# Kernel tuning notes

Measured on AMD Instinct MI355X. Metric: run time of the kernel, lower is better.

## Reference

```python
import jax, jax.numpy as jnp
import numpy as np

N = 4096        # nodes
E = 131072      # edges (avg degree 32)
IN_F = 256      # in_features
OUT_F = 64      # out_features per head
H = 8           # num_heads


def setup_inputs() -> dict:
    key = jax.random.key(0)
    k1, k2, k3, k4 = jax.random.split(key, 4)
    x = jax.random.normal(k1, (N, IN_F), dtype=jnp.float32)
    # xavier-ish scales for the learned params
    W = jax.random.normal(k2, (IN_F, OUT_F * H), dtype=jnp.float32) * 0.06
    a = jax.random.normal(k3, (2 * OUT_F, 1), dtype=jnp.float32) * 0.12
    edge_index = jax.random.randint(k4, (2, E), 0, N, dtype=jnp.int32)
    return {"x": x, "W": W, "a": a, "edge_index": edge_index}


def reference(x, W, a, edge_index):
    n = x.shape[0]
    Wh = (x @ W).reshape(n, H, OUT_F)          # [N, H, F]
    src, dst = edge_index[0], edge_index[1]
    # edge score: cat(Wh[src], Wh[dst]) @ a == Wh[src]@a1 + Wh[dst]@a2
    a1 = a[:OUT_F, 0]                           # [F]
    a2 = a[OUT_F:2 * OUT_F, 0]                  # [F]
    alpha_src = Wh @ a1                         # [N, H]
    alpha_dst = Wh @ a2                         # [N, H]
    edge_e = jax.nn.leaky_relu(alpha_src[src] + alpha_dst[dst], 0.2)  # [E, H]
    # dense scatter exactly as the original module (non-edges stay 0 in softmax)
    attention = jnp.zeros((n, n, H), dtype=x.dtype).at[src, dst].set(edge_e)
    attention = jax.nn.softmax(attention, axis=1)
    # dropout is identity in eval mode
    h_prime = jnp.einsum('nmh,mhf->nhf', attention, Wh)  # [N, H, F]
    return h_prime.reshape(n, H * OUT_F)        # concat=True
```

## Files before the change

### kernel.cpp

```cpp
#include <hip/hip_runtime.h>
#include <hip/hip_bf16.h>

constexpr int NN    = 4096;
constexpr int EE    = 131072;
constexpr int IN_F  = 256;
constexpr int OUT_F = 64;
constexpr int HH    = 8;
constexpr int HF    = OUT_F * HH;
constexpr int CAP   = 128;

__device__ __forceinline__ unsigned short f2b(float f) {
    unsigned int u = __float_as_uint(f);
    u = u + 0x7FFFu + ((u >> 16) & 1u);
    return (unsigned short)(u >> 16);
}
__device__ __forceinline__ float b2f(unsigned int lo16) {
    return __uint_as_float(lo16 << 16);
}

#define TM 64
#define TN 64
#define TK 32

__global__ __launch_bounds__(256) void gemm_fused(const float* __restrict__ x,
                                                  const float* __restrict__ W,
                                                  const float* __restrict__ a,
                                                  unsigned short* __restrict__ Whb,
                                                  float* __restrict__ asrc,
                                                  float* __restrict__ adst,
                                                  float* __restrict__ S) {
    __shared__ float As[TK][TM + 4];
    __shared__ float Bs[TK][TN + 4];
    __shared__ float Scol[TN];
    int t  = threadIdx.x;
    int tx = t & 15;
    int ty = t >> 4;
    int m0 = blockIdx.x * TM;
    int n0 = blockIdx.y * TN;
    float acc[4][4] = {};

    float4 pa[2], pb[2];
    {
#pragma unroll
        for (int i = 0; i < 2; ++i) {
            int flat = i * 256 + t, row = flat >> 3, c4 = flat & 7;
            pa[i] = *(const float4*)(x + (size_t)(m0 + row) * IN_F + c4 * 4);
        }
#pragma unroll
        for (int i = 0; i < 2; ++i) {
            int flat = i * 256 + t, row = flat >> 4, c4 = flat & 15;
            pb[i] = *(const float4*)(W + (size_t)row * HF + n0 + c4 * 4);
        }
    }

    for (int k0 = 0; k0 < IN_F; k0 += TK) {
#pragma unroll
        for (int i = 0; i < 2; ++i) {
            int flat = i * 256 + t, row = flat >> 3, c4 = flat & 7;
            As[c4 * 4 + 0][row] = pa[i].x;
            As[c4 * 4 + 1][row] = pa[i].y;
            As[c4 * 4 + 2][row] = pa[i].z;
            As[c4 * 4 + 3][row] = pa[i].w;
        }
#pragma unroll
        for (int i = 0; i < 2; ++i) {
            int flat = i * 256 + t, row = flat >> 4, c4 = flat & 15;
            *(float4*)(&Bs[row][c4 * 4]) = pb[i];
        }
        __syncthreads();
        if (k0 + TK < IN_F) {
            int kn = k0 + TK;
#pragma unroll
            for (int i = 0; i < 2; ++i) {
                int flat = i * 256 + t, row = flat >> 3, c4 = flat & 7;
                pa[i] = *(const float4*)(x + (size_t)(m0 + row) * IN_F + kn + c4 * 4);
            }
#pragma unroll
            for (int i = 0; i < 2; ++i) {
                int flat = i * 256 + t, row = flat >> 4, c4 = flat & 15;
                pb[i] = *(const float4*)(W + (size_t)(kn + row) * HF + n0 + c4 * 4);
            }
        }
#pragma unroll
        for (int k = 0; k < TK; ++k) {
            float4 a4 = *(const float4*)(&As[k][ty * 4]);
            float4 b4 = *(const float4*)(&Bs[k][tx * 4]);
            float av[4] = {a4.x, a4.y, a4.z, a4.w};
            float bv[4] = {b4.x, b4.y, b4.z, b4.w};
#pragma unroll
            for (int ii = 0; ii < 4; ++ii)
#pragma unroll
                for (int jj = 0; jj < 4; ++jj)
                    acc[ii][jj] += av[ii] * bv[jj];
        }
        __syncthreads();
    }

#pragma unroll
    for (int ii = 0; ii < 4; ++ii) {
        ushort4 v;
        v.x = f2b(acc[ii][0]);
        v.y = f2b(acc[ii][1]);
        v.z = f2b(acc[ii][2]);
        v.w = f2b(acc[ii][3]);
        *(ushort4*)(Whb + (size_t)(m0 + ty * 4 + ii) * HF + n0 + tx * 4) = v;
    }

    int h = n0 >> 6;
    float a1v[4], a2v[4];
#pragma unroll
    for (int jj = 0; jj < 4; ++jj) {
        int f = tx * 4 + jj;
        a1v[jj] = a[f];
        a2v[jj] = a[OUT_F + f];
    }
#pragma unroll
    for (int ii = 0; ii < 4; ++ii) {
        float p1 = 0.f, p2 = 0.f;
#pragma unroll
        for (int jj = 0; jj < 4; ++jj) {
            p1 += acc[ii][jj] * a1v[jj];
            p2 += acc[ii][jj] * a2v[jj];
        }
#pragma unroll
        for (int mask = 1; mask < 16; mask <<= 1) {
            p1 += __shfl_xor(p1, mask);
            p2 += __shfl_xor(p2, mask);
        }
        if (tx == 0) {
            int node = m0 + ty * 4 + ii;
            asrc[node * HH + h] = p1;
            adst[node * HH + h] = p2;
        }
    }

    if (t < TN) Scol[t] = 0.f;
    __syncthreads();
#pragma unroll
    for (int jj = 0; jj < 4; ++jj) {
        float cs = acc[0][jj] + acc[1][jj] + acc[2][jj] + acc[3][jj];
        atomicAdd(&Scol[tx * 4 + jj], cs);
    }
    __syncthreads();
    if (t < TN) atomicAdd(&S[n0 + t], Scol[t]);
}

__global__ __launch_bounds__(256) void scatter_lite(const int* __restrict__ src,
                                                    const int* __restrict__ dst,
                                                    int* __restrict__ cnt,
                                                    int* __restrict__ csr_dst) {
    int e = blockIdx.x * 256 + threadIdx.x;
    if (e >= EE) return;
    int s = src[e], d = dst[e];
    int pos = atomicAdd(&cnt[s], 1);
    csr_dst[(s << 7) + pos] = d;
}

__global__ __launch_bounds__(512) void aggregate_kernel(const unsigned short* __restrict__ Whb,
                                                        const float* __restrict__ asrc,
                                                        const float* __restrict__ adst,
                                                        const float* __restrict__ S,
                                                        const int* __restrict__ cnt,
                                                        const int* __restrict__ csr_dst,
                                                        float* __restrict__ out) {
    __shared__ int           midx[CAP];
    __shared__ unsigned char dupf[CAP];
    __shared__ float         wbuf[CAP * HH];
    __shared__ float         as_sh[HH];
    __shared__ float         denom[HH];
    __shared__ float         red[8][HF];
    int i = blockIdx.x;
    int t = threadIdx.x;
    int deg = cnt[i];
    if (deg > CAP) deg = CAP;

    if (t < HH) as_sh[t] = asrc[i * HH + t];
    for (int j = t; j < deg; j += 512) midx[j] = csr_dst[(i << 7) + j];
    __syncthreads();

    for (int j = t; j < deg; j += 512) {
        int m = midx[j];
        unsigned char f = 0;
        for (int k = 0; k < j; ++k)
            if (midx[k] == m) { f = 1; break; }
        dupf[j] = f;
    }
    __syncthreads();

    for (int idx = t; idx < deg * HH; idx += 512) {
        int sl = idx >> 3, h = idx & 7;
        float w = 0.f;
        if (!dupf[sl]) {
            float xv = as_sh[h] + adst[midx[sl] * HH + h];
            xv = (xv > 0.f) ? xv : 0.2f * xv;
            w = __expf(xv) - 1.f;
        }
        wbuf[idx] = w;
    }
    __syncthreads();

    if (t < 128) {
        int h = t >> 4, ln = t & 15;
        float p = 0.f;
        for (int sl = ln; sl < deg; sl += 16) p += wbuf[sl * HH + h];
#pragma unroll
        for (int mask = 1; mask < 16; mask <<= 1) p += __shfl_xor(p, mask);
        if (ln == 0) denom[h] = (float)NN + p;
    }
    __syncthreads();

    int g = t >> 6;
    int r = t & 63;
    int h = r >> 3;
    float accv[8] = {};

    int j = g;
    uint4 uC = {0, 0, 0, 0};
    float wC = 0.f;
    if (j < deg) {
        wC = wbuf[j * HH + h];
        uC = *(const uint4*)(Whb + ((size_t)midx[j] << 9) + (r << 3));
    }
    while (j < deg) {
        int jn = j + 8;
        uint4 uN = {0, 0, 0, 0};
        float wN = 0.f;
        if (jn < deg) {
            wN = wbuf[jn * HH + h];
            uN = *(const uint4*)(Whb + ((size_t)midx[jn] << 9) + (r << 3));
        }
        accv[0] += wC * b2f(uC.x & 0xFFFFu);
        accv[1] += wC * b2f(uC.x >> 16);
        accv[2] += wC * b2f(uC.y & 0xFFFFu);
        accv[3] += wC * b2f(uC.y >> 16);
        accv[4] += wC * b2f(uC.z & 0xFFFFu);
        accv[5] += wC * b2f(uC.z >> 16);
        accv[6] += wC * b2f(uC.w & 0xFFFFu);
        accv[7] += wC * b2f(uC.w >> 16);
        uC = uN; wC = wN; j = jn;
    }

    float4 v0 = {accv[0], accv[1], accv[2], accv[3]};
    float4 v1 = {accv[4], accv[5], accv[6], accv[7]};
    *(float4*)(&red[g][r * 8])     = v0;
    *(float4*)(&red[g][r * 8 + 4]) = v1;
    __syncthreads();

    float tot = S[t];
#pragma unroll
    for (int gg = 0; gg < 8; ++gg) tot += red[gg][t];
    out[((size_t)i << 9) + t] = tot / denom[t >> 6];
}

extern "C" void kernel_launch(void* const* d_in, const int* in_sizes, int n_in,
                              void* d_out, int out_size, void* d_ws, size_t ws_size,
                              hipStream_t stream) {
    const float* x  = (const float*)d_in[0];
    const float* W  = (const float*)d_in[1];
    const float* a  = (const float*)d_in[2];
    const int*   ei = (const int*)d_in[3];
    const int* src = ei;
    const int* dst = ei + EE;
    float* out = (float*)d_out;

    char* ws = (char*)d_ws;
    unsigned short* Whb = (unsigned short*)(ws + 0);
    float* asrc     = (float*)(ws + 4194304);
    float* adst     = (float*)(ws + 4325376);
    int*   csr_dst  = (int*)  (ws + 4456448);
    float* S        = (float*)(ws + 6553600);
    int*   cnt      = (int*)  (ws + 6555648);

    hipMemsetAsync(ws + 6553600, 0, 2048 + 16384, stream);

    scatter_lite<<<EE / 256, 256, 0, stream>>>(src, dst, cnt, csr_dst);

    gemm_fused<<<dim3(NN / TM, HF / TN), 256, 0, stream>>>(x, W, a, Whb, asrc, adst, S);

    aggregate_kernel<<<NN, 512, 0, stream>>>(Whb, asrc, adst, S, cnt, csr_dst, out);
}
```

Before: 132.3 us.

## Fuse memset, scatter, GEMM and aggregation into one cooperative persistent kernel

Replaces the memset plus three separate kernel launches with a single cooperative kernel of 512 blocks × 256 threads that uses grid-wide syncs between phases: zeroing, CSR scatter, the fused GEMM, and the per-node aggregation. The aggregation phase becomes a persistent loop where each block handles 8 nodes with 4 gather groups instead of 8. This removes launch gaps and inter-kernel overhead. In exchange it adds grid barrier costs, and the aggregation gets less parallelism per node and fewer concurrent waves to hide gather latency.

Result: slower. 320.4 us (+142.3%).

```diff
diff --git a/kernel.cpp b/kernel.cpp
--- a/kernel.cpp
+++ b/kernel.cpp
@@ -1,5 +1,8 @@
 #include <hip/hip_runtime.h>
 #include <hip/hip_bf16.h>
+#include <hip/hip_cooperative_groups.h>
+
+namespace cg = cooperative_groups;
 
 constexpr int NN    = 4096;
 constexpr int EE    = 131072;
@@ -9,6 +12,9 @@
 constexpr int HF    = OUT_F * HH;
 constexpr int CAP   = 128;
 
+constexpr int GRID  = 512;
+constexpr int BLK   = 256;
+
 __device__ __forceinline__ unsigned short f2b(float f) {
     unsigned int u = __float_as_uint(f);
     u = u + 0x7FFFu + ((u >> 16) & 1u);
@@ -22,25 +28,45 @@
 #define TN 64
 #define TK 32
 
-__global__ __launch_bounds__(256) void gemm_fused(const float* __restrict__ x,
-                                                  const float* __restrict__ W,
-                                                  const float* __restrict__ a,
-                                                  unsigned short* __restrict__ Whb,
-                                                  float* __restrict__ asrc,
-                                                  float* __restrict__ adst,
-                                                  float* __restrict__ S) {
-    __shared__ float As[TK][TM + 4];
-    __shared__ float Bs[TK][TN + 4];
-    __shared__ float Scol[TN];
-    int t  = threadIdx.x;
-    int tx = t & 15;
-    int ty = t >> 4;
-    int m0 = blockIdx.x * TM;
-    int n0 = blockIdx.y * TN;
-    float acc[4][4] = {};
-
-    float4 pa[2], pb[2];
+__global__ __launch_bounds__(BLK) void gat_mega(const float* __restrict__ x,
+                                                const float* __restrict__ W,
+                                                const float* __restrict__ a,
+                                                const int* __restrict__ src,
+                                                const int* __restrict__ dst,
+                                                unsigned short* __restrict__ Whb,
+                                                float* __restrict__ asrc,
+                                                float* __restrict__ adst,
+                                                float* __restrict__ S,
+                                                int* __restrict__ cnt,
+                                                int* __restrict__ csr_dst,
+                                                float* __restrict__ out) {
+    cg::grid_group grid = cg::this_grid();
+    int b = blockIdx.x;
+    int t = threadIdx.x;
+    int gt = b * BLK + t;
+
+    if (gt < NN) cnt[gt] = 0;
+    if (gt >= NN && gt < NN + HF) S[gt - NN] = 0.f;
+    grid.sync();
+
     {
+        int s = src[gt], d = dst[gt];
+        int pos = atomicAdd(&cnt[s], 1);
+        csr_dst[(s << 7) + pos] = d;
+    }
+    grid.sync();
+
+    {
+        __shared__ float As[TK][TM + 4];
+        __shared__ float Bs[TK][TN + 4];
+        __shared__ float Scol[TN];
+        int tx = t & 15;
+        int ty = t >> 4;
+        int m0 = (b >> 3) * TM;
+        int n0 = (b & 7) * TN;
+        float acc[4][4] = {};
+
+        float4 pa[2], pb[2];
 #pragma unroll
         for (int i = 0; i < 2; ++i) {
             int flat = i * 256 + t, row = flat >> 3, c4 = flat & 7;
@@ -51,205 +77,191 @@
             int flat = i * 256 + t, row = flat >> 4, c4 = flat & 15;
             pb[i] = *(const float4*)(W + (size_t)row * HF + n0 + c4 * 4);
         }
-    }
-
-    for (int k0 = 0; k0 < IN_F; k0 += TK) {
-#pragma unroll
-        for (int i = 0; i < 2; ++i) {
-            int flat = i * 256 + t, row = flat >> 3, c4 = flat & 7;
-            As[c4 * 4 + 0][row] = pa[i].x;
-            As[c4 * 4 + 1][row] = pa[i].y;
-            As[c4 * 4 + 2][row] = pa[i].z;
-            As[c4 * 4 + 3][row] = pa[i].w;
-        }
-#pragma unroll
-        for (int i = 0; i < 2; ++i) {
-            int flat = i * 256 + t, row = flat >> 4, c4 = flat & 15;
-            *(float4*)(&Bs[row][c4 * 4]) = pb[i];
-        }
-        __syncthreads();
-        if (k0 + TK < IN_F) {
-            int kn = k0 + TK;
+
+        for (int k0 = 0; k0 < IN_F; k0 += TK) {
 #pragma unroll
             for (int i = 0; i < 2; ++i) {
                 int flat = i * 256 + t, row = flat >> 3, c4 = flat & 7;
-                pa[i] = *(const float4*)(x + (size_t)(m0 + row) * IN_F + kn + c4 * 4);
+                As[c4 * 4 + 0][row] = pa[i].x;
+                As[c4 * 4 + 1][row] = pa[i].y;
+                As[c4 * 4 + 2][row] = pa[i].z;
+                As[c4 * 4 + 3][row] = pa[i].w;
             }
 #pragma unroll
             for (int i = 0; i < 2; ++i) {
                 int flat = i * 256 + t, row = flat >> 4, c4 = flat & 15;
-                pb[i] = *(const float4*)(W + (size_t)(kn + row) * HF + n0 + c4 * 4);
-            }
-        }
-#pragma unroll
-        for (int k = 0; k < TK; ++k) {
-            float4 a4 = *(const float4*)(&As[k][ty * 4]);
-            float4 b4 = *(const float4*)(&Bs[k][tx * 4]);
-            float av[4] = {a4.x, a4.y, a4.z, a4.w};
-            float bv[4] = {b4.x, b4.y, b4.z, b4.w};
-#pragma unroll
-            for (int ii = 0; ii < 4; ++ii)
-#pragma unroll
-                for (int jj = 0; jj < 4; ++jj)
-                    acc[ii][jj] += av[ii] * bv[jj];
-        }
+                *(float4*)(&Bs[row][c4 * 4]) = pb[i];
+            }
+            __syncthreads();
+            if (k0 + TK < IN_F) {
+                int kn = k0 + TK;
+#pragma unroll
+                for (int i = 0; i < 2; ++i) {
+                    int flat = i * 256 + t, row = flat >> 3, c4 = flat & 7;
+                    pa[i] = *(const float4*)(x + (size_t)(m0 + row) * IN_F + kn + c4 * 4);
+                }
+#pragma unroll
+                for (int i = 0; i < 2; ++i) {
+                    int flat = i * 256 + t, row = flat >> 4, c4 = flat & 15;
+                    pb[i] = *(const float4*)(W + (size_t)(kn + row) * HF + n0 + c4 * 4);
+                }
+            }
+#pragma unroll
+            for (int k = 0; k < TK; ++k) {
+                float4 a4 = *(const float4*)(&As[k][ty * 4]);
+                float4 b4 = *(const float4*)(&Bs[k][tx * 4]);
+                float av[4] = {a4.x, a4.y, a4.z, a4.w};
+                float bv[4] = {b4.x, b4.y, b4.z, b4.w};
+#pragma unroll
+                for (int ii = 0; ii < 4; ++ii)
+#pragma unroll
+                    for (int jj = 0; jj < 4; ++jj)
+                        acc[ii][jj] += av[ii] * bv[jj];
+            }
+            __syncthreads();
+        }
+
+#pragma unroll
+        for (int ii = 0; ii < 4; ++ii) {
+            ushort4 v;
+            v.x = f2b(acc[ii][0]);
+            v.y = f2b(acc[ii][1]);
+            v.z = f2b(acc[ii][2]);
+            v.w = f2b(acc[ii][3]);
+            *(ushort4*)(Whb + (size_t)(m0 + ty * 4 + ii) * HF + n0 + tx * 4) = v;
+        }
+
+        int h = n0 >> 6;
+        float a1v[4], a2v[4];
+#pragma unroll
+        for (int jj = 0; jj < 4; ++jj) {
+            int f = tx * 4 + jj;
+            a1v[jj] = a[f];
+            a2v[jj] = a[OUT_F + f];
+        }
+#pragma unroll
+        for (int ii = 0; ii < 4; ++ii) {
+            float p1 = 0.f, p2 = 0.f;
+#pragma unroll
+            for (int jj = 0; jj < 4; ++jj) {
+                p1 += acc[ii][jj] * a1v[jj];
+                p2 += acc[ii][jj] * a2v[jj];
+            }
+#pragma unroll
+            for (int mask = 1; mask < 16; mask <<= 1) {
+                p1 += __shfl_xor(p1, mask);
+                p2 += __shfl_xor(p2, mask);
+            }
+            if (tx == 0) {
+                int node = m0 + ty * 4 + ii;
+                asrc[node * HH + h] = p1;
+                adst[node * HH + h] = p2;
+            }
+        }
+
+        if (t < TN) Scol[t] = 0.f;
         __syncthreads();
+#pragma unroll
+        for (int jj = 0; jj < 4; ++jj) {
+            float cs = acc[0][jj] + acc[1][jj] + acc[2][jj] + acc[3][jj];
+            atomicAdd(&Scol[tx * 4 + jj], cs);
+        }
+        __syncthreads();
+        if (t < TN) atomicAdd(&S[n0 + t], Scol[t]);
     }
-
-#pragma unroll
-    for (int ii = 0; ii < 4; ++ii) {
-        ushort4 v;
-        v.x = f2b(acc[ii][0]);
-        v.y = f2b(acc[ii][1]);
-        v.z = f2b(acc[ii][2]);
-        v.w = f2b(acc[ii][3]);
-        *(ushort4*)(Whb + (size_t)(m0 + ty * 4 + ii) * HF + n0 + tx * 4) = v;
+    grid.sync();
+
+    {
+        __shared__ int           midx[CAP];
+        __shared__ unsigned char dupf[CAP];
+        __shared__ float         wbuf[CAP * HH];
+        __shared__ float         as_sh[HH];
+        __shared__ float         denom[HH];
+        __shared__ float         red[4][HF];
+
+        for (int i = b; i < NN; i += GRID) {
+            int deg = cnt[i];
+            if (deg > CAP) deg = CAP;
+
+            if (t < HH) as_sh[t] = asrc[i * HH + t];
+            for (int j = t; j < deg; j += BLK) midx[j] = csr_dst[(i << 7) + j];
+            __syncthreads();
+
+            for (int j = t; j < deg; j += BLK) {
+                int m = midx[j];
+                unsigned char f = 0;
+                for (int k = 0; k < j; ++k)
+                    if (midx[k] == m) { f = 1; break; }
+                dupf[j] = f;
+            }
+            __syncthreads();
+
+            for (int idx = t; idx < deg * HH; idx += BLK) {
+                int sl = idx >> 3, h = idx & 7;
+                float w = 0.f;
+                if (!dupf[sl]) {
+                    float xv = as_sh[h] + adst[midx[sl] * HH + h];
+                    xv = (xv > 0.f) ? xv : 0.2f * xv;
+                    w = __expf(xv) - 1.f;
+                }
+                wbuf[idx] = w;
+            }
+            __syncthreads();
+
+            if (t < 128) {
+                int h = t >> 4, ln = t & 15;
+                float p = 0.f;
+                for (int sl = ln; sl < deg; sl += 16) p += wbuf[sl * HH + h];
+#pragma unroll
+                for (int mask = 1; mask < 16; mask <<= 1) p += __shfl_xor(p, mask);
+                if (ln == 0) denom[h] = (float)NN + p;
+            }
+            __syncthreads();
+
+            int g = t >> 6;
+            int r = t & 63;
+            int h = r >> 3;
+            float accv[8] = {};
+
+            int j = g;
+            uint4 uC = {0, 0, 0, 0};
+            float wC = 0.f;
+            if (j < deg) {
+                wC = wbuf[j * HH + h];
+                uC = *(const uint4*)(Whb + ((size_t)midx[j] << 9) + (r << 3));
+            }
+            while (j < deg) {
+                int jn = j + 4;
+                uint4 uN = {0, 0, 0, 0};
+                float wN = 0.f;
+                if (jn < deg) {
+                    wN = wbuf[jn * HH + h];
+                    uN = *(const uint4*)(Whb + ((size_t)midx[jn] << 9) + (r << 3));
+                }
+                accv[0] += wC * b2f(uC.x & 0xFFFFu);
+                accv[1] += wC * b2f(uC.x >> 16);
+                accv[2] += wC * b2f(uC.y & 0xFFFFu);
+                accv[3] += wC * b2f(uC.y >> 16);
+                accv[4] += wC * b2f(uC.z & 0xFFFFu);
+                accv[5] += wC * b2f(uC.z >> 16);
+                accv[6] += wC * b2f(uC.w & 0xFFFFu);
+                accv[7] += wC * b2f(uC.w >> 16);
+                uC = uN; wC = wN; j = jn;
+            }
+
+            float4 v0 = {accv[0], accv[1], accv[2], accv[3]};
+            float4 v1 = {accv[4], accv[5], accv[6], accv[7]};
+            *(float4*)(&red[g][r * 8])     = v0;
+            *(float4*)(&red[g][r * 8 + 4]) = v1;
+            __syncthreads();
+
+            for (int o = t; o < HF; o += BLK) {
+                float tot = S[o] + red[0][o] + red[1][o] + red[2][o] + red[3][o];
+                out[((size_t)i << 9) + o] = tot / denom[o >> 6];
+            }
+            __syncthreads();
+        }
     }
-
-    int h = n0 >> 6;
-    float a1v[4], a2v[4];
-#pragma unroll
-    for (int jj = 0; jj < 4; ++jj) {
-        int f = tx * 4 + jj;
-        a1v[jj] = a[f];
-        a2v[jj] = a[OUT_F + f];
-    }
-#pragma unroll
-    for (int ii = 0; ii < 4; ++ii) {
-        float p1 = 0.f, p2 = 0.f;
-#pragma unroll
-        for (int jj = 0; jj < 4; ++jj) {
-            p1 += acc[ii][jj] * a1v[jj];
-            p2 += acc[ii][jj] * a2v[jj];
-        }
-#pragma unroll
-        for (int mask = 1; mask < 16; mask <<= 1) {
-            p1 += __shfl_xor(p1, mask);
-            p2 += __shfl_xor(p2, mask);
-        }
-        if (tx == 0) {
-            int node = m0 + ty * 4 + ii;
-            asrc[node * HH + h] = p1;
-            adst[node * HH + h] = p2;
-        }
-    }
-
-    if (t < TN) Scol[t] = 0.f;
-    __syncthreads();
-#pragma unroll
-    for (int jj = 0; jj < 4; ++jj) {
-        float cs = acc[0][jj] + acc[1][jj] + acc[2][jj] + acc[3][jj];
-        atomicAdd(&Scol[tx * 4 + jj], cs);
-    }
-    __syncthreads();
-    if (t < TN) atomicAdd(&S[n0 + t], Scol[t]);
-}
-
-__global__ __launch_bounds__(256) void scatter_lite(const int* __restrict__ src,
-                                                    const int* __restrict__ dst,
-                                                    int* __restrict__ cnt,
-                                                    int* __restrict__ csr_dst) {
-    int e = blockIdx.x * 256 + threadIdx.x;
-    if (e >= EE) return;
-    int s = src[e], d = dst[e];
-    int pos = atomicAdd(&cnt[s], 1);
-    csr_dst[(s << 7) + pos] = d;
-}
-
-__global__ __launch_bounds__(512) void aggregate_kernel(const unsigned short* __restrict__ Whb,
-                                                        const float* __restrict__ asrc,
-                                                        const float* __restrict__ adst,
-                                                        const float* __restrict__ S,
-                                                        const int* __restrict__ cnt,
-                                                        const int* __restrict__ csr_dst,
-                                                        float* __restrict__ out) {
-    __shared__ int           midx[CAP];
-    __shared__ unsigned char dupf[CAP];
-    __shared__ float         wbuf[CAP * HH];
-    __shared__ float         as_sh[HH];
-    __shared__ float         denom[HH];
-    __shared__ float         red[8][HF];
-    int i = blockIdx.x;
-    int t = threadIdx.x;
-    int deg = cnt[i];
-    if (deg > CAP) deg = CAP;
-
-    if (t < HH) as_sh[t] = asrc[i * HH + t];
-    for (int j = t; j < deg; j += 512) midx[j] = csr_dst[(i << 7) + j];
-    __syncthreads();
-
-    for (int j = t; j < deg; j += 512) {
-        int m = midx[j];
-        unsigned char f = 0;
-        for (int k = 0; k < j; ++k)
-            if (midx[k] == m) { f = 1; break; }
-        dupf[j] = f;
-    }
-    __syncthreads();
-
-    for (int idx = t; idx < deg * HH; idx += 512) {
-        int sl = idx >> 3, h = idx & 7;
-        float w = 0.f;
-        if (!dupf[sl]) {
-            float xv = as_sh[h] + adst[midx[sl] * HH + h];
-            xv = (xv > 0.f) ? xv : 0.2f * xv;
-            w = __expf(xv) - 1.f;
-        }
-        wbuf[idx] = w;
-    }
-    __syncthreads();
-
-    if (t < 128) {
-        int h = t >> 4, ln = t & 15;
-        float p = 0.f;
-        for (int sl = ln; sl < deg; sl += 16) p += wbuf[sl * HH + h];
-#pragma unroll
-        for (int mask = 1; mask < 16; mask <<= 1) p += __shfl_xor(p, mask);
-        if (ln == 0) denom[h] = (float)NN + p;
-    }
-    __syncthreads();
-
-    int g = t >> 6;
-    int r = t & 63;
-    int h = r >> 3;
-    float accv[8] = {};
-
-    int j = g;
-    uint4 uC = {0, 0, 0, 0};
-    float wC = 0.f;
-    if (j < deg) {
-        wC = wbuf[j * HH + h];
-        uC = *(const uint4*)(Whb + ((size_t)midx[j] << 9) + (r << 3));
-    }
-    while (j < deg) {
-        int jn = j + 8;
-        uint4 uN = {0, 0, 0, 0};
-        float wN = 0.f;
-        if (jn < deg) {
-            wN = wbuf[jn * HH + h];
-            uN = *(const uint4*)(Whb + ((size_t)midx[jn] << 9) + (r << 3));
-        }
-        accv[0] += wC * b2f(uC.x & 0xFFFFu);
-        accv[1] += wC * b2f(uC.x >> 16);
-        accv[2] += wC * b2f(uC.y & 0xFFFFu);
-        accv[3] += wC * b2f(uC.y >> 16);
-        accv[4] += wC * b2f(uC.z & 0xFFFFu);
-        accv[5] += wC * b2f(uC.z >> 16);
-        accv[6] += wC * b2f(uC.w & 0xFFFFu);
-        accv[7] += wC * b2f(uC.w >> 16);
-        uC = uN; wC = wN; j = jn;
-    }
-
-    float4 v0 = {accv[0], accv[1], accv[2], accv[3]};
-    float4 v1 = {accv[4], accv[5], accv[6], accv[7]};
-    *(float4*)(&red[g][r * 8])     = v0;
-    *(float4*)(&red[g][r * 8 + 4]) = v1;
-    __syncthreads();
-
-    float tot = S[t];
-#pragma unroll
-    for (int gg = 0; gg < 8; ++gg) tot += red[gg][t];
-    out[((size_t)i << 9) + t] = tot / denom[t >> 6];
 }
 
 extern "C" void kernel_launch(void* const* d_in, const int* in_sizes, int n_in,
@@ -271,11 +283,9 @@
     float* S        = (float*)(ws + 6553600);
     int*   cnt      = (int*)  (ws + 6555648);
 
-    hipMemsetAsync(ws + 6553600, 0, 2048 + 16384, stream);
-
-    scatter_lite<<<EE / 256, 256, 0, stream>>>(src, dst, cnt, csr_dst);
-
-    gemm_fused<<<dim3(NN / TM, HF / TN), 256, 0, stream>>>(x, W, a, Whb, asrc, adst, S);
-
-    aggregate_kernel<<<NN, 512, 0, stream>>>(Whb, asrc, adst, S, cnt, csr_dst, out);
-}
+    void* args[] = {(void*)&x, (void*)&W, (void*)&a, (void*)&src, (void*)&dst,
+                    (void*)&Whb, (void*)&asrc, (void*)&adst, (void*)&S,
+                    (void*)&cnt, (void*)&csr_dst, (void*)&out};
+    hipLaunchCooperativeKernel((const void*)gat_mega, dim3(GRID), dim3(BLK),
+                               args, 0, stream);
+}
```

## Fuse edge scatter into GEMM kernel and double-buffer shared tiles

Applied to the files above, without the earlier changes.

Merges the separate CSR-scatter kernel into the projection GEMM, so each of the 512 GEMM blocks also handles 256 edges, which removes one kernel launch. The GEMM's shared-memory tiles are now double-buffered, which drops one barrier per k-step. The cost is double the LDS usage, which may reduce occupancy. The fused grid only works because blocks times threads exactly equals the edge count.

New measurement: 128.3 us. 3.0% less time.

```diff
diff --git a/kernel.cpp b/kernel.cpp
--- a/kernel.cpp
+++ b/kernel.cpp
@@ -22,54 +22,66 @@
 #define TN 64
 #define TK 32
 
-__global__ __launch_bounds__(256) void gemm_fused(const float* __restrict__ x,
-                                                  const float* __restrict__ W,
-                                                  const float* __restrict__ a,
-                                                  unsigned short* __restrict__ Whb,
-                                                  float* __restrict__ asrc,
-                                                  float* __restrict__ adst,
-                                                  float* __restrict__ S) {
-    __shared__ float As[TK][TM + 4];
-    __shared__ float Bs[TK][TN + 4];
+__global__ __launch_bounds__(256) void gemm_scatter(const float* __restrict__ x,
+                                                    const float* __restrict__ W,
+                                                    const float* __restrict__ a,
+                                                    const int* __restrict__ src,
+                                                    const int* __restrict__ dst,
+                                                    int* __restrict__ cnt,
+                                                    int* __restrict__ csr_dst,
+                                                    unsigned short* __restrict__ Whb,
+                                                    float* __restrict__ asrc,
+                                                    float* __restrict__ adst,
+                                                    float* __restrict__ S) {
+    __shared__ float As[2][TK][TM + 4];
+    __shared__ float Bs[2][TK][TN + 4];
     __shared__ float Scol[TN];
-    int t  = threadIdx.x;
+    int b = blockIdx.x;
+    int t = threadIdx.x;
+
+    {
+        int e = b * 256 + t;
+        int s = src[e], d = dst[e];
+        int pos = atomicAdd(&cnt[s], 1);
+        csr_dst[(s << 7) + pos] = d;
+    }
+
     int tx = t & 15;
     int ty = t >> 4;
-    int m0 = blockIdx.x * TM;
-    int n0 = blockIdx.y * TN;
+    int m0 = (b >> 3) * TM;
+    int n0 = (b & 7) * TN;
     float acc[4][4] = {};
-
     float4 pa[2], pb[2];
-    {
-#pragma unroll
-        for (int i = 0; i < 2; ++i) {
-            int flat = i * 256 + t, row = flat >> 3, c4 = flat & 7;
-            pa[i] = *(const float4*)(x + (size_t)(m0 + row) * IN_F + c4 * 4);
-        }
-#pragma unroll
-        for (int i = 0; i < 2; ++i) {
-            int flat = i * 256 + t, row = flat >> 4, c4 = flat & 15;
-            pb[i] = *(const float4*)(W + (size_t)row * HF + n0 + c4 * 4);
-        }
-    }
-
-    for (int k0 = 0; k0 < IN_F; k0 += TK) {
-#pragma unroll
-        for (int i = 0; i < 2; ++i) {
-            int flat = i * 256 + t, row = flat >> 3, c4 = flat & 7;
-            As[c4 * 4 + 0][row] = pa[i].x;
-            As[c4 * 4 + 1][row] = pa[i].y;
-            As[c4 * 4 + 2][row] = pa[i].z;
-            As[c4 * 4 + 3][row] = pa[i].w;
-        }
-#pragma unroll
-        for (int i = 0; i < 2; ++i) {
-            int flat = i * 256 + t, row = flat >> 4, c4 = flat & 15;
-            *(float4*)(&Bs[row][c4 * 4]) = pb[i];
-        }
-        __syncthreads();
-        if (k0 + TK < IN_F) {
-            int kn = k0 + TK;
+
+#pragma unroll
+    for (int i = 0; i < 2; ++i) {
+        int flat = i * 256 + t, row = flat >> 3, c4 = flat & 7;
+        pa[i] = *(const float4*)(x + (size_t)(m0 + row) * IN_F + c4 * 4);
+    }
+#pragma unroll
+    for (int i = 0; i < 2; ++i) {
+        int flat = i * 256 + t, row = flat >> 4, c4 = flat & 15;
+        pb[i] = *(const float4*)(W + (size_t)row * HF + n0 + c4 * 4);
+    }
+#pragma unroll
+    for (int i = 0; i < 2; ++i) {
+        int flat = i * 256 + t, row = flat >> 3, c4 = flat & 7;
+        As[0][c4 * 4 + 0][row] = pa[i].x;
+        As[0][c4 * 4 + 1][row] = pa[i].y;
+        As[0][c4 * 4 + 2][row] = pa[i].z;
+        As[0][c4 * 4 + 3][row] = pa[i].w;
+    }
+#pragma unroll
+    for (int i = 0; i < 2; ++i) {
+        int flat = i * 256 + t, row = flat >> 4, c4 = flat & 15;
+        *(float4*)(&Bs[0][row][c4 * 4]) = pb[i];
+    }
+    __syncthreads();
+
+    for (int s8 = 0; s8 < 8; ++s8) {
+        int cur = s8 & 1;
+        if (s8 < 7) {
+            int kn = (s8 + 1) * TK;
 #pragma unroll
             for (int i = 0; i < 2; ++i) {
                 int flat = i * 256 + t, row = flat >> 3, c4 = flat & 7;
@@ -83,8 +95,8 @@
         }
 #pragma unroll
         for (int k = 0; k < TK; ++k) {
-            float4 a4 = *(const float4*)(&As[k][ty * 4]);
-            float4 b4 = *(const float4*)(&Bs[k][tx * 4]);
+            float4 a4 = *(const float4*)(&As[cur][k][ty * 4]);
+            float4 b4 = *(const float4*)(&Bs[cur][k][tx * 4]);
             float av[4] = {a4.x, a4.y, a4.z, a4.w};
             float bv[4] = {b4.x, b4.y, b4.z, b4.w};
 #pragma unroll
@@ -93,7 +105,23 @@
                 for (int jj = 0; jj < 4; ++jj)
                     acc[ii][jj] += av[ii] * bv[jj];
         }
-        __syncthreads();
+        if (s8 < 7) {
+            int nxt = cur ^ 1;
+#pragma unroll
+            for (int i = 0; i < 2; ++i) {
+                int flat = i * 256 + t, row = flat >> 3, c4 = flat & 7;
+                As[nxt][c4 * 4 + 0][row] = pa[i].x;
+                As[nxt][c4 * 4 + 1][row] = pa[i].y;
+                As[nxt][c4 * 4 + 2][row] = pa[i].z;
+                As[nxt][c4 * 4 + 3][row] = pa[i].w;
+            }
+#pragma unroll
+            for (int i = 0; i < 2; ++i) {
+                int flat = i * 256 + t, row = flat >> 4, c4 = flat & 15;
+                *(float4*)(&Bs[nxt][row][c4 * 4]) = pb[i];
+            }
+            __syncthreads();
+        }
     }
 
 #pragma unroll
@@ -143,17 +171,6 @@
     }
     __syncthreads();
     if (t < TN) atomicAdd(&S[n0 + t], Scol[t]);
-}
-
-__global__ __launch_bounds__(256) void scatter_lite(const int* __restrict__ src,
-                                                    const int* __restrict__ dst,
-                                                    int* __restrict__ cnt,
-                                                    int* __restrict__ csr_dst) {
-    int e = blockIdx.x * 256 + threadIdx.x;
-    if (e >= EE) return;
-    int s = src[e], d = dst[e];
-    int pos = atomicAdd(&cnt[s], 1);
-    csr_dst[(s << 7) + pos] = d;
 }
 
 __global__ __launch_bounds__(512) void aggregate_kernel(const unsigned short* __restrict__ Whb,
@@ -273,9 +290,8 @@
 
     hipMemsetAsync(ws + 6553600, 0, 2048 + 16384, stream);
 
-    scatter_lite<<<EE / 256, 256, 0, stream>>>(src, dst, cnt, csr_dst);
-
-    gemm_fused<<<dim3(NN / TM, HF / TN), 256, 0, stream>>>(x, W, a, Whb, asrc, adst, S);
+    gemm_scatter<<<512, 256, 0, stream>>>(x, W, a, src, dst, cnt, csr_dst,
+                                          Whb, asrc, adst, S);
 
     aggregate_kernel<<<NN, 512, 0, stream>>>(Whb, asrc, adst, S, cnt, csr_dst, out);
 }
```

## Use split-bf16 MFMA GEMM with preconversion and fuse edge scatter into GEMM

Applied to the files above, without the earlier changes.

Replaces the fp32 SIMT GEMM with bf16 MFMA instructions, splitting x and W into hi/lo bf16 parts (three MFMAs per tile) to keep near-fp32 accuracy. A new preconvert kernel does the hi/lo split, transposes W, and zeroes the counters, which replaces the memset. The CSR edge scatter moves into the GEMM kernel, so one launch goes away. The cost is the extra passes that write and read the converted copies, plus the scatter atomics now running inside the GEMM blocks.

Result: faster. 119.1 us (-9.9%).

```diff
diff --git a/kernel.cpp b/kernel.cpp
--- a/kernel.cpp
+++ b/kernel.cpp
@@ -9,6 +9,9 @@
 constexpr int HF    = OUT_F * HH;
 constexpr int CAP   = 128;
 
+typedef __attribute__((ext_vector_type(8))) short bf16x8;
+typedef __attribute__((ext_vector_type(4))) float f32x4;
+
 __device__ __forceinline__ unsigned short f2b(float f) {
     unsigned int u = __float_as_uint(f);
     u = u + 0x7FFFu + ((u >> 16) & 1u);
@@ -18,142 +21,161 @@
     return __uint_as_float(lo16 << 16);
 }
 
-#define TM 64
-#define TN 64
-#define TK 32
-
-__global__ __launch_bounds__(256) void gemm_fused(const float* __restrict__ x,
+__global__ __launch_bounds__(256) void preconvert(const float* __restrict__ x,
                                                   const float* __restrict__ W,
-                                                  const float* __restrict__ a,
-                                                  unsigned short* __restrict__ Whb,
-                                                  float* __restrict__ asrc,
-                                                  float* __restrict__ adst,
-                                                  float* __restrict__ S) {
-    __shared__ float As[TK][TM + 4];
-    __shared__ float Bs[TK][TN + 4];
-    __shared__ float Scol[TN];
-    int t  = threadIdx.x;
-    int tx = t & 15;
-    int ty = t >> 4;
-    int m0 = blockIdx.x * TM;
-    int n0 = blockIdx.y * TN;
-    float acc[4][4] = {};
-
-    float4 pa[2], pb[2];
+                                                  unsigned short* __restrict__ xhi,
+                                                  unsigned short* __restrict__ xlo,
+                                                  unsigned short* __restrict__ WThi,
+                                                  unsigned short* __restrict__ WTlo,
+                                                  float* __restrict__ S,
+                                                  int* __restrict__ cnt) {
+    int b = blockIdx.x, t = threadIdx.x;
+    if (b < 512) {
+        int base = (b * 256 + t) * 8;
+        float4 v0 = *(const float4*)(x + base);
+        float4 v1 = *(const float4*)(x + base + 4);
+        float f[8] = {v0.x, v0.y, v0.z, v0.w, v1.x, v1.y, v1.z, v1.w};
+        unsigned short hi[8], lo[8];
+#pragma unroll
+        for (int j = 0; j < 8; ++j) {
+            hi[j] = f2b(f[j]);
+            lo[j] = f2b(f[j] - b2f(hi[j]));
+        }
+        *(ushort4*)(xhi + base)     = make_ushort4(hi[0], hi[1], hi[2], hi[3]);
+        *(ushort4*)(xhi + base + 4) = make_ushort4(hi[4], hi[5], hi[6], hi[7]);
+        *(ushort4*)(xlo + base)     = make_ushort4(lo[0], lo[1], lo[2], lo[3]);
+        *(ushort4*)(xlo + base + 4) = make_ushort4(lo[4], lo[5], lo[6], lo[7]);
+    } else {
+        int bb = b - 512;
+        int gt2 = bb * 256 + t;
+        if (gt2 < NN) cnt[gt2] = 0;
+        else if (gt2 < NN + HF) S[gt2 - NN] = 0.f;
+        int n  = bb * 8 + (t >> 5);
+        int kb = (t & 31) * 8;
+        unsigned short hi[8], lo[8];
+#pragma unroll
+        for (int j = 0; j < 8; ++j) {
+            float f = W[(size_t)(kb + j) * HF + n];
+            hi[j] = f2b(f);
+            lo[j] = f2b(f - b2f(hi[j]));
+        }
+        size_t o = (size_t)n * 256 + kb;
+        *(ushort4*)(WThi + o)     = make_ushort4(hi[0], hi[1], hi[2], hi[3]);
+        *(ushort4*)(WThi + o + 4) = make_ushort4(hi[4], hi[5], hi[6], hi[7]);
+        *(ushort4*)(WTlo + o)     = make_ushort4(lo[0], lo[1], lo[2], lo[3]);
+        *(ushort4*)(WTlo + o + 4) = make_ushort4(lo[4], lo[5], lo[6], lo[7]);
+    }
+}
+
+__global__ __launch_bounds__(256) void gemm_mfma(const unsigned short* __restrict__ xhi,
+                                                 const unsigned short* __restrict__ xlo,
+                                                 const unsigned short* __restrict__ WThi,
+                                                 const unsigned short* __restrict__ WTlo,
+                                                 const float* __restrict__ a,
+                                                 const int* __restrict__ src,
+                                                 const int* __restrict__ dst,
+                                                 int* __restrict__ cnt,
+                                                 int* __restrict__ csr_dst,
+                                                 unsigned short* __restrict__ Whb,
+                                                 float* __restrict__ asrc,
+                                                 float* __restrict__ adst,
+                                                 float* __restrict__ S) {
+    __shared__ unsigned short Bhi_s[64][264];
+    __shared__ unsigned short Blo_s[64][264];
+    __shared__ float Scol[64];
+    int b = blockIdx.x;
+    int t = threadIdx.x;
+
     {
-#pragma unroll
-        for (int i = 0; i < 2; ++i) {
-            int flat = i * 256 + t, row = flat >> 3, c4 = flat & 7;
-            pa[i] = *(const float4*)(x + (size_t)(m0 + row) * IN_F + c4 * 4);
-        }
-#pragma unroll
-        for (int i = 0; i < 2; ++i) {
-            int flat = i * 256 + t, row = flat >> 4, c4 = flat & 15;
-            pb[i] = *(const float4*)(W + (size_t)row * HF + n0 + c4 * 4);
-        }
-    }
-
-    for (int k0 = 0; k0 < IN_F; k0 += TK) {
-#pragma unroll
-        for (int i = 0; i < 2; ++i) {
-            int flat = i * 256 + t, row = flat >> 3, c4 = flat & 7;
-            As[c4 * 4 + 0][row] = pa[i].x;
-            As[c4 * 4 + 1][row] = pa[i].y;
-            As[c4 * 4 + 2][row] = pa[i].z;
-            As[c4 * 4 + 3][row] = pa[i].w;
-        }
-#pragma unroll
-        for (int i = 0; i < 2; ++i) {
-            int flat = i * 256 + t, row = flat >> 4, c4 = flat & 15;
-            *(float4*)(&Bs[row][c4 * 4]) = pb[i];
-        }
-        __syncthreads();
-        if (k0 + TK < IN_F) {
-            int kn = k0 + TK;
-#pragma unroll
-            for (int i = 0; i < 2; ++i) {
-                int flat = i * 256 + t, row = flat >> 3, c4 = flat & 7;
-                pa[i] = *(const float4*)(x + (size_t)(m0 + row) * IN_F + kn + c4 * 4);
-            }
-#pragma unroll
-            for (int i = 0; i < 2; ++i) {
-                int flat = i * 256 + t, row = flat >> 4, c4 = flat & 15;
-                pb[i] = *(const float4*)(W + (size_t)(kn + row) * HF + n0 + c4 * 4);
-            }
-        }
-#pragma unroll
-        for (int k = 0; k < TK; ++k) {
-            float4 a4 = *(const float4*)(&As[k][ty * 4]);
-            float4 b4 = *(const float4*)(&Bs[k][tx * 4]);
-            float av[4] = {a4.x, a4.y, a4.z, a4.w};
-            float bv[4] = {b4.x, b4.y, b4.z, b4.w};
-#pragma unroll
-            for (int ii = 0; ii < 4; ++ii)
-#pragma unroll
-                for (int jj = 0; jj < 4; ++jj)
-                    acc[ii][jj] += av[ii] * bv[jj];
-        }
-        __syncthreads();
-    }
-
-#pragma unroll
-    for (int ii = 0; ii < 4; ++ii) {
-        ushort4 v;
-        v.x = f2b(acc[ii][0]);
-        v.y = f2b(acc[ii][1]);
-        v.z = f2b(acc[ii][2]);
-        v.w = f2b(acc[ii][3]);
-        *(ushort4*)(Whb + (size_t)(m0 + ty * 4 + ii) * HF + n0 + tx * 4) = v;
-    }
+        int e = b * 256 + t;
+        int s = src[e], d = dst[e];
+        int pos = atomicAdd(&cnt[s], 1);
+        csr_dst[(s << 7) + pos] = d;
+    }
+
+    int m0 = (b >> 3) * 64;
+    int n0 = (b & 7) * 64;
+    if (t < 64) Scol[t] = 0.f;
+
+#pragma unroll
+    for (int it = 0; it < 8; ++it) {
+        int flat = it * 256 + t;
+        int row  = flat >> 5;
+        int cu   = flat & 31;
+        *(uint4*)(&Bhi_s[row][cu * 8]) =
+            *(const uint4*)(WThi + (size_t)(n0 + row) * 256 + cu * 8);
+        *(uint4*)(&Blo_s[row][cu * 8]) =
+            *(const uint4*)(WTlo + (size_t)(n0 + row) * 256 + cu * 8);
+    }
+    __syncthreads();
+
+    int w  = t >> 6;
+    int l  = t & 63;
+    int kg = l >> 4;
+    int ln = l & 15;
+    int arow = m0 + w * 16 + ln;
+
+    f32x4 acc[4] = {};
+
+#pragma unroll
+    for (int ks = 0; ks < 8; ++ks) {
+        size_t aoff = (size_t)arow * 256 + ks * 32 + kg * 8;
+        bf16x8 ahi = *(const bf16x8*)(xhi + aoff);
+        bf16x8 alo = *(const bf16x8*)(xlo + aoff);
+#pragma unroll
+        for (int nt = 0; nt < 4; ++nt) {
+            const unsigned short* bp = &Bhi_s[nt * 16 + ln][ks * 32 + kg * 8];
+            const unsigned short* lp = &Blo_s[nt * 16 + ln][ks * 32 + kg * 8];
+            bf16x8 bhi = *(const bf16x8*)bp;
+            bf16x8 blo = *(const bf16x8*)lp;
+            acc[nt] = __builtin_amdgcn_mfma_f32_16x16x32_bf16(ahi, bhi, acc[nt], 0, 0, 0);
+            acc[nt] = __builtin_amdgcn_mfma_f32_16x16x32_bf16(ahi, blo, acc[nt], 0, 0, 0);
+            acc[nt] = __builtin_amdgcn_mfma_f32_16x16x32_bf16(alo, bhi, acc[nt], 0, 0, 0);
+        }
+    }
+
+#pragma unroll
+    for (int nt = 0; nt < 4; ++nt)
+#pragma unroll
+        for (int i = 0; i < 4; ++i) {
+            int row = m0 + w * 16 + kg * 4 + i;
+            Whb[(size_t)row * HF + n0 + nt * 16 + ln] = f2b(acc[nt][i]);
+        }
 
     int h = n0 >> 6;
     float a1v[4], a2v[4];
 #pragma unroll
-    for (int jj = 0; jj < 4; ++jj) {
-        int f = tx * 4 + jj;
-        a1v[jj] = a[f];
-        a2v[jj] = a[OUT_F + f];
-    }
-#pragma unroll
-    for (int ii = 0; ii < 4; ++ii) {
-        float p1 = 0.f, p2 = 0.f;
-#pragma unroll
-        for (int jj = 0; jj < 4; ++jj) {
-            p1 += acc[ii][jj] * a1v[jj];
-            p2 += acc[ii][jj] * a2v[jj];
-        }
+    for (int nt = 0; nt < 4; ++nt) {
+        a1v[nt] = a[nt * 16 + ln];
+        a2v[nt] = a[OUT_F + nt * 16 + ln];
+    }
+#pragma unroll
+    for (int i = 0; i < 4; ++i) {
+        float p1 = acc[0][i] * a1v[0] + acc[1][i] * a1v[1] +
+                   acc[2][i] * a1v[2] + acc[3][i] * a1v[3];
+        float p2 = acc[0][i] * a2v[0] + acc[1][i] * a2v[1] +
+                   acc[2][i] * a2v[2] + acc[3][i] * a2v[3];
 #pragma unroll
         for (int mask = 1; mask < 16; mask <<= 1) {
             p1 += __shfl_xor(p1, mask);
             p2 += __shfl_xor(p2, mask);
         }
-        if (tx == 0) {
-            int node = m0 + ty * 4 + ii;
+        if (ln == 0) {
+            int node = m0 + w * 16 + kg * 4 + i;
             asrc[node * HH + h] = p1;
             adst[node * HH + h] = p2;
         }
     }
 
-    if (t < TN) Scol[t] = 0.f;
-    __syncthreads();
-#pragma unroll
-    for (int jj = 0; jj < 4; ++jj) {
-        float cs = acc[0][jj] + acc[1][jj] + acc[2][jj] + acc[3][jj];
-        atomicAdd(&Scol[tx * 4 + jj], cs);
-    }
-    __syncthreads();
-    if (t < TN) atomicAdd(&S[n0 + t], Scol[t]);
-}
-
-__global__ __launch_bounds__(256) void scatter_lite(const int* __restrict__ src,
-                                                    const int* __restrict__ dst,
-                                                    int* __restrict__ cnt,
-                                                    int* __restrict__ csr_dst) {
-    int e = blockIdx.x * 256 + threadIdx.x;
-    if (e >= EE) return;
-    int s = src[e], d = dst[e];
-    int pos = atomicAdd(&cnt[s], 1);
-    csr_dst[(s << 7) + pos] = d;
+#pragma unroll
+    for (int nt = 0; nt < 4; ++nt) {
+        float cs = acc[nt][0] + acc[nt][1] + acc[nt][2] + acc[nt][3];
+        cs += __shfl_xor(cs, 16);
+        cs += __shfl_xor(cs, 32);
+        if (kg == 0) atomicAdd(&Scol[nt * 16 + ln], cs);
+    }
+    __syncthreads();
+    if (t < 64) atomicAdd(&S[n0 + t], Scol[t]);
 }
 
 __global__ __launch_bounds__(512) void aggregate_kernel(const unsigned short* __restrict__ Whb,
@@ -264,18 +286,21 @@
     float* out = (float*)d_out;
 
     char* ws = (char*)d_ws;
-    unsigned short* Whb = (unsigned short*)(ws + 0);
-    float* asrc     = (float*)(ws + 4194304);
-    float* adst     = (float*)(ws + 4325376);
-    int*   csr_dst  = (int*)  (ws + 4456448);
-    float* S        = (float*)(ws + 6553600);
-    int*   cnt      = (int*)  (ws + 6555648);
-
-    hipMemsetAsync(ws + 6553600, 0, 2048 + 16384, stream);
-
-    scatter_lite<<<EE / 256, 256, 0, stream>>>(src, dst, cnt, csr_dst);
-
-    gemm_fused<<<dim3(NN / TM, HF / TN), 256, 0, stream>>>(x, W, a, Whb, asrc, adst, S);
+    unsigned short* Whb  = (unsigned short*)(ws + 0);
+    unsigned short* xhi  = (unsigned short*)(ws + 4194304);
+    unsigned short* xlo  = (unsigned short*)(ws + 6291456);
+    unsigned short* WThi = (unsigned short*)(ws + 8388608);
+    unsigned short* WTlo = (unsigned short*)(ws + 8650752);
+    float* asrc     = (float*)(ws + 8912896);
+    float* adst     = (float*)(ws + 9043968);
+    int*   csr_dst  = (int*)  (ws + 9175040);
+    float* S        = (float*)(ws + 11272192);
+    int*   cnt      = (int*)  (ws + 11274240);
+
+    preconvert<<<576, 256, 0, stream>>>(x, W, xhi, xlo, WThi, WTlo, S, cnt);
+
+    gemm_mfma<<<512, 256, 0, stream>>>(xhi, xlo, WThi, WTlo, a, src, dst,
+                                       cnt, csr_dst, Whb, asrc, adst, S);
 
     aggregate_kernel<<<NN, 512, 0, stream>>>(Whb, asrc, adst, S, cnt, csr_dst, out);
 }
```
